# Optimization experiments

Hardware: AMD Instinct MI355X
Metric: run time of the kernel (lower is better)

Reference implementation:

```python
import jax, jax.numpy as jnp
import numpy as np

B, H, S, DK = 2, 16, 2048, 64


def setup_inputs() -> dict:
    key = jax.random.key(0)
    kq, kk, kv = jax.random.split(key, 3)
    query = jax.random.normal(kq, (B, H, S, DK), dtype=jnp.float32)
    k = jax.random.normal(kk, (B, H, S, DK), dtype=jnp.float32)
    value = jax.random.normal(kv, (B, H, S, DK), dtype=jnp.float32)
    # causal padding-style mask: 1 = keep, 0 = masked (set to -inf pre-softmax)
    mask = jnp.tril(jnp.ones((S, S), dtype=jnp.int32))[None, None, :, :]
    return {"query": query, "key": k, "value": value, "d_k": DK, "mask": mask}


def reference(query, key, value, d_k, mask):
    # scores: [B, H, Sq, Sk]
    scores = jnp.einsum("bhqd,bhkd->bhqk", query, key)
    scores = scores / jnp.sqrt(jnp.asarray(d_k, dtype=scores.dtype))
    scores = jnp.where(mask == 0, -jnp.inf, scores)
    att = jax.nn.softmax(scores, axis=-1)
    # dropout is identity in eval mode (deterministic reference)
    out = jnp.einsum("bhqk,bhkd->bhqd", att, value)
    return out
```

## Files before the change

kernel.cpp:

```cpp
#include <hip/hip_runtime.h>
#include <cstdint>

#define B_ 2
#define H_ 16
#define S_ 2048
#define DK_ 64
#define BH_ (B_*H_)
#define NQT 32

typedef __attribute__((ext_vector_type(8))) short short8;
typedef __attribute__((ext_vector_type(4))) float floatx4;
typedef __attribute__((ext_vector_type(16))) float floatx16;

__device__ inline unsigned short f2bf(float f) {
  union { float f; unsigned u; } v; v.f = f;
  unsigned u = v.u;
  unsigned r = u + 0x7fffu + ((u >> 16) & 1u);
  return (unsigned short)(r >> 16);
}

__device__ inline floatx16 mfma32(short8 a, short8 b, floatx16 c) {
  return __builtin_amdgcn_mfma_f32_32x32x16_bf16(a, b, c, 0, 0, 0);
}

__global__ __launch_bounds__(256) void conv_kv(const float* __restrict__ K,
                                               const float* __restrict__ V,
                                               unsigned short* __restrict__ Kb,
                                               unsigned short* __restrict__ Vb) {
  __shared__ __align__(16) unsigned short t[64 * 80];
  const int bh = blockIdx.y, s0 = blockIdx.x * 64;
  const int row = threadIdx.x >> 2, cp = threadIdx.x & 3;

  {
    const float* src = K + ((size_t)(bh * S_ + s0 + row)) * DK_ + cp * 16;
    unsigned short* dst = Kb + ((size_t)(bh * S_ + s0 + row)) * DK_ + cp * 16;
    #pragma unroll
    for (int h = 0; h < 2; ++h) {
      float4 a = *(const float4*)(src + h * 8);
      float4 b = *(const float4*)(src + h * 8 + 4);
      uint4 st;
      st.x = (unsigned)f2bf(a.x) | ((unsigned)f2bf(a.y) << 16);
      st.y = (unsigned)f2bf(a.z) | ((unsigned)f2bf(a.w) << 16);
      st.z = (unsigned)f2bf(b.x) | ((unsigned)f2bf(b.y) << 16);
      st.w = (unsigned)f2bf(b.z) | ((unsigned)f2bf(b.w) << 16);
      *(uint4*)(dst + h * 8) = st;
    }
  }
  {
    const float* src = V + ((size_t)(bh * S_ + s0 + row)) * DK_ + cp * 16;
    #pragma unroll
    for (int j4 = 0; j4 < 4; ++j4) {
      float4 a = *(const float4*)(src + j4 * 4);
      int c = cp * 16 + j4 * 4;
      t[(c + 0) * 80 + row] = f2bf(a.x);
      t[(c + 1) * 80 + row] = f2bf(a.y);
      t[(c + 2) * 80 + row] = f2bf(a.z);
      t[(c + 3) * 80 + row] = f2bf(a.w);
    }
    __syncthreads();
    unsigned short* dst = Vb + ((size_t)(bh * DK_ + row)) * S_ + s0 + cp * 16;
    *(uint4*)(dst + 0) = *(const uint4*)&t[row * 80 + cp * 16];
    *(uint4*)(dst + 8) = *(const uint4*)&t[row * 80 + cp * 16 + 8];
  }
}

__global__ __launch_bounds__(256, 4)
void fa_kernel(const float* __restrict__ Q, const unsigned short* __restrict__ Kb,
               const unsigned short* __restrict__ Vb, float* __restrict__ Out) {
  __shared__ __align__(16) unsigned short SMEM[2 * 8192 + 256];

  const int tid  = threadIdx.x;
  const int wave = tid >> 6;
  const int lane = tid & 63;
  const int l31  = lane & 31;
  const int h    = lane >> 5;
  const int wq   = wave >> 1;
  const int ws   = wave & 1;

  const int id = blockIdx.x;
  const int bh = id & 31;
  const int u  = id >> 5;
  const int r  = u & 7, k4 = u >> 3;
  const int qt = (k4 == 0) ? r : (k4 == 1) ? (15 - r) : (k4 == 2) ? (16 + r) : (31 - r);
  const int nkv = qt + 1;

  const float SCL = 0.125f * 1.44269504088896340736f;

  short8 qf[4];
  {
    const float* qp = Q + ((size_t)bh * S_ + qt * 64 + wq * 32 + l31) * DK_ + h * 8;
    #pragma unroll
    for (int dstep = 0; dstep < 4; ++dstep) {
      float4 x = *(const float4*)(qp + dstep * 16);
      float4 y = *(const float4*)(qp + dstep * 16 + 4);
      short8 t;
      t[0]=(short)f2bf(x.x*SCL); t[1]=(short)f2bf(x.y*SCL); t[2]=(short)f2bf(x.z*SCL); t[3]=(short)f2bf(x.w*SCL);
      t[4]=(short)f2bf(y.x*SCL); t[5]=(short)f2bf(y.y*SCL); t[6]=(short)f2bf(y.z*SCL); t[7]=(short)f2bf(y.w*SCL);
      qf[dstep] = t;
    }
  }

  floatx16 Ot[2] = { {0,0,0,0,0,0,0,0,0,0,0,0,0,0,0,0},
                     {0,0,0,0,0,0,0,0,0,0,0,0,0,0,0,0} };
  float ls = 0.f;

  auto stage = [&](int slot, int kv) {
    #pragma unroll
    for (int rd = 0; rd < 2; ++rd) {
      const int cid = rd * 256 + tid;
      const int row = cid >> 3;
      const int c   = (cid & 7) ^ (row & 7);
      {
        const unsigned short* g = Kb + (((size_t)bh * S_ + kv * 64 + row) << 6) + (c << 3);
        __builtin_amdgcn_global_load_lds(
            (const __attribute__((address_space(1))) void*)g,
            (__attribute__((address_space(3))) void*)&SMEM[slot * 8192 + rd * 2048 + wave * 512],
            16, 0, 0);
      }
      {
        const unsigned short* g = Vb + (((size_t)(bh * DK_ + row)) << 11) + kv * 64 + (c << 3);
        __builtin_amdgcn_global_load_lds(
            (const __attribute__((address_space(1))) void*)g,
            (__attribute__((address_space(3))) void*)&SMEM[slot * 8192 + 4096 + rd * 2048 + wave * 512],
            16, 0, 0);
      }
    }
  };

  auto computeT = [&](int cur, bool diag) {
    if (diag && wq == 0 && ws == 1) return;
    const unsigned short* Kt = SMEM + cur * 8192;
    const unsigned short* Vt = Kt + 4096;
    floatx16 s = {0,0,0,0,0,0,0,0,0,0,0,0,0,0,0,0};
    const int krow = ws * 32 + l31;
    #pragma unroll
    for (int dstep = 0; dstep < 4; ++dstep) {
      const short8 a = *(const short8*)&Kt[krow * 64 + (((dstep << 1) + h) ^ (krow & 7)) * 8];
      s = mfma32(a, qf[dstep], s);
    }
    if (diag && wq == ws) {
      #pragma unroll
      for (int rg = 0; rg < 16; ++rg) {
        const int sl = (rg & 3) + 8 * (rg >> 2) + 4 * h;
        if (sl > l31) s[rg] = -INFINITY;
      }
    }
    float e[16];
    #pragma unroll
    for (int i = 0; i < 16; ++i) e[i] = __builtin_amdgcn_exp2f(s[i]);
    ls += (((e[0]+e[1])+(e[2]+e[3])) + ((e[4]+e[5])+(e[6]+e[7])))
        + (((e[8]+e[9])+(e[10]+e[11])) + ((e[12]+e[13])+(e[14]+e[15])));
    short8 pb[2];
    #pragma unroll
    for (int t = 0; t < 2; ++t) {
      unsigned X0, X1, Y0, Y1;
      asm("v_cvt_pk_bf16_f32 %0, %1, %2" : "=v"(X0) : "v"(e[8*t+0]), "v"(e[8*t+1]));
      asm("v_cvt_pk_bf16_f32 %0, %1, %2" : "=v"(X1) : "v"(e[8*t+2]), "v"(e[8*t+3]));
      asm("v_cvt_pk_bf16_f32 %0, %1, %2" : "=v"(Y0) : "v"(e[8*t+4]), "v"(e[8*t+5]));
      asm("v_cvt_pk_bf16_f32 %0, %1, %2" : "=v"(Y1) : "v"(e[8*t+6]), "v"(e[8*t+7]));
      asm("v_permlane32_swap_b32 %0, %1" : "+v"(X0), "+v"(Y0));
      asm("v_permlane32_swap_b32 %0, %1" : "+v"(X1), "+v"(Y1));
      union { unsigned u[4]; short8 s8; } pbu;
      pbu.u[0] = X0; pbu.u[1] = X1; pbu.u[2] = Y0; pbu.u[3] = Y1;
      pb[t] = pbu.s8;
    }
    #pragma unroll
    for (int dsub = 0; dsub < 2; ++dsub) {
      const int vrow = dsub * 32 + l31;
      const short8 v0 = *(const short8*)&Vt[vrow * 64 + (((ws << 2) + h    ) ^ (vrow & 7)) * 8];
      const short8 v1 = *(const short8*)&Vt[vrow * 64 + (((ws << 2) + h + 2) ^ (vrow & 7)) * 8];
      Ot[dsub] = mfma32(v0, pb[0], Ot[dsub]);
      Ot[dsub] = mfma32(v1, pb[1], Ot[dsub]);
    }
  };

  stage(0, 0);
  for (int kv = 0; kv < nkv; ++kv) {
    asm volatile("s_waitcnt vmcnt(0)" ::: "memory");
    __builtin_amdgcn_s_barrier();
    if (kv + 1 < nkv) stage((kv + 1) & 1, kv + 1);
    computeT(kv & 1, kv == nkv - 1);
  }

  ls += __shfl_xor(ls, 32);
  float* OP = (float*)SMEM;
  float* LP = OP + 4096;
  __syncthreads();
  if (ws == 1) {
    #pragma unroll
    for (int dsub = 0; dsub < 2; ++dsub)
      #pragma unroll
      for (int rg = 0; rg < 16; ++rg)
        OP[((wq * 2 + dsub) * 16 + rg) * 64 + lane] = Ot[dsub][rg];
    LP[wq * 64 + lane] = ls;
  }
  __syncthreads();
  if (ws == 0) {
    const float inv = 1.0f / (ls + LP[wq * 64 + lane]);
    float* og = Out + ((size_t)(bh * S_ + qt * 64 + wq * 32 + l31)) * DK_;
    #pragma unroll
    for (int dsub = 0; dsub < 2; ++dsub) {
      #pragma unroll
      for (int g = 0; g < 4; ++g) {
        floatx4 o;
        #pragma unroll
        for (int j = 0; j < 4; ++j)
          o[j] = (Ot[dsub][4 * g + j] + OP[((wq * 2 + dsub) * 16 + 4 * g + j) * 64 + lane]) * inv;
        *(floatx4*)(og + dsub * 32 + 8 * g + 4 * h) = o;
      }
    }
  }
}

extern "C" void kernel_launch(void* const* d_in, const int* in_sizes, int n_in,
                              void* d_out, int out_size, void* d_ws, size_t ws_size,
                              hipStream_t stream) {
  const float* Q = (const float*)d_in[0];
  const float* K = (const float*)d_in[1];
  const float* V = (const float*)d_in[2];
  float* Out = (float*)d_out;
  unsigned short* Kb = (unsigned short*)d_ws;
  unsigned short* Vb = Kb + (size_t)BH_ * S_ * DK_;
  conv_kv<<<dim3(S_ / 64, BH_), 256, 0, stream>>>(K, V, Kb, Vb);
  fa_kernel<<<dim3(NQT * BH_), 256, 0, stream>>>(Q, Kb, Vb, Out);
}
```

Baseline: 131.9 us.

## Pair complementary causal query tiles per block to share K/V tile loads

Each workgroup now processes two query tiles (p and 31-p), so every block does the same amount of causal work, and the K/V tiles staged in LDS plus the fragments read from them are reused by both tiles. The change halves the grid, cuts global and LDS traffic for K/V per unit of work, and removes the imbalance between short and long causal rows. In exchange register pressure roughly doubles for the Q fragments and accumulators, so launch bounds drop to 2 blocks per CU. There are also only 512 blocks, which may leave the GPU with less latency hiding.

After: 131.7 us. Within noise of the previous version (-0.1%).

```diff
diff --git a/kernel.cpp b/kernel.cpp
--- a/kernel.cpp
+++ b/kernel.cpp
@@ -64,7 +64,7 @@
   }
 }
 
-__global__ __launch_bounds__(256, 4)
+__global__ __launch_bounds__(256, 2)
 void fa_kernel(const float* __restrict__ Q, const unsigned short* __restrict__ Kb,
                const unsigned short* __restrict__ Vb, float* __restrict__ Out) {
   __shared__ __align__(16) unsigned short SMEM[2 * 8192 + 256];
@@ -79,15 +79,14 @@
 
   const int id = blockIdx.x;
   const int bh = id & 31;
-  const int u  = id >> 5;
-  const int r  = u & 7, k4 = u >> 3;
-  const int qt = (k4 == 0) ? r : (k4 == 1) ? (15 - r) : (k4 == 2) ? (16 + r) : (31 - r);
-  const int nkv = qt + 1;
+  const int p  = id >> 5;
+  const int qa = p, qb = NQT - 1 - p;
+  const int nkvA = qa + 1, nkvB = qb + 1;
 
   const float SCL = 0.125f * 1.44269504088896340736f;
 
-  short8 qf[4];
-  {
+  short8 qfB[4], qfA[4];
+  auto loadQ = [&](int qt, short8* qf) {
     const float* qp = Q + ((size_t)bh * S_ + qt * 64 + wq * 32 + l31) * DK_ + h * 8;
     #pragma unroll
     for (int dstep = 0; dstep < 4; ++dstep) {
@@ -98,11 +97,15 @@
       t[4]=(short)f2bf(y.x*SCL); t[5]=(short)f2bf(y.y*SCL); t[6]=(short)f2bf(y.z*SCL); t[7]=(short)f2bf(y.w*SCL);
       qf[dstep] = t;
     }
-  }
-
-  floatx16 Ot[2] = { {0,0,0,0,0,0,0,0,0,0,0,0,0,0,0,0},
-                     {0,0,0,0,0,0,0,0,0,0,0,0,0,0,0,0} };
-  float ls = 0.f;
+  };
+  loadQ(qb, qfB);
+  loadQ(qa, qfA);
+
+  floatx16 OtB[2] = { {0,0,0,0,0,0,0,0,0,0,0,0,0,0,0,0},
+                      {0,0,0,0,0,0,0,0,0,0,0,0,0,0,0,0} };
+  floatx16 OtA[2] = { {0,0,0,0,0,0,0,0,0,0,0,0,0,0,0,0},
+                      {0,0,0,0,0,0,0,0,0,0,0,0,0,0,0,0} };
+  float lsB = 0.f, lsA = 0.f;
 
   auto stage = [&](int slot, int kv) {
     #pragma unroll
@@ -127,17 +130,12 @@
     }
   };
 
-  auto computeT = [&](int cur, bool diag) {
+  auto doTile = [&](const short8* ak, const short8 (*vf)[2], const short8* qf,
+                    floatx16* Ot, float& ls, bool diag) {
     if (diag && wq == 0 && ws == 1) return;
-    const unsigned short* Kt = SMEM + cur * 8192;
-    const unsigned short* Vt = Kt + 4096;
     floatx16 s = {0,0,0,0,0,0,0,0,0,0,0,0,0,0,0,0};
-    const int krow = ws * 32 + l31;
-    #pragma unroll
-    for (int dstep = 0; dstep < 4; ++dstep) {
-      const short8 a = *(const short8*)&Kt[krow * 64 + (((dstep << 1) + h) ^ (krow & 7)) * 8];
-      s = mfma32(a, qf[dstep], s);
-    }
+    #pragma unroll
+    for (int dstep = 0; dstep < 4; ++dstep) s = mfma32(ak[dstep], qf[dstep], s);
     if (diag && wq == ws) {
       #pragma unroll
       for (int rg = 0; rg < 16; ++rg) {
@@ -166,49 +164,70 @@
     }
     #pragma unroll
     for (int dsub = 0; dsub < 2; ++dsub) {
-      const int vrow = dsub * 32 + l31;
-      const short8 v0 = *(const short8*)&Vt[vrow * 64 + (((ws << 2) + h    ) ^ (vrow & 7)) * 8];
-      const short8 v1 = *(const short8*)&Vt[vrow * 64 + (((ws << 2) + h + 2) ^ (vrow & 7)) * 8];
-      Ot[dsub] = mfma32(v0, pb[0], Ot[dsub]);
-      Ot[dsub] = mfma32(v1, pb[1], Ot[dsub]);
+      Ot[dsub] = mfma32(vf[dsub][0], pb[0], Ot[dsub]);
+      Ot[dsub] = mfma32(vf[dsub][1], pb[1], Ot[dsub]);
     }
   };
 
   stage(0, 0);
-  for (int kv = 0; kv < nkv; ++kv) {
+  for (int kv = 0; kv < nkvB; ++kv) {
     asm volatile("s_waitcnt vmcnt(0)" ::: "memory");
     __builtin_amdgcn_s_barrier();
-    if (kv + 1 < nkv) stage((kv + 1) & 1, kv + 1);
-    computeT(kv & 1, kv == nkv - 1);
-  }
-
-  ls += __shfl_xor(ls, 32);
+    if (kv + 1 < nkvB) stage((kv + 1) & 1, kv + 1);
+    const unsigned short* Kt = SMEM + (kv & 1) * 8192;
+    const unsigned short* Vt = Kt + 4096;
+    short8 ak[4];
+    const int krow = ws * 32 + l31;
+    #pragma unroll
+    for (int dstep = 0; dstep < 4; ++dstep)
+      ak[dstep] = *(const short8*)&Kt[krow * 64 + (((dstep << 1) + h) ^ (krow & 7)) * 8];
+    short8 vf[2][2];
+    #pragma unroll
+    for (int dsub = 0; dsub < 2; ++dsub) {
+      const int vrow = dsub * 32 + l31;
+      vf[dsub][0] = *(const short8*)&Vt[vrow * 64 + (((ws << 2) + h    ) ^ (vrow & 7)) * 8];
+      vf[dsub][1] = *(const short8*)&Vt[vrow * 64 + (((ws << 2) + h + 2) ^ (vrow & 7)) * 8];
+    }
+    doTile(ak, vf, qfB, OtB, lsB, kv == nkvB - 1);
+    if (kv < nkvA) doTile(ak, vf, qfA, OtA, lsA, kv == nkvA - 1);
+  }
+
+  lsB += __shfl_xor(lsB, 32);
+  lsA += __shfl_xor(lsA, 32);
+
   float* OP = (float*)SMEM;
   float* LP = OP + 4096;
   __syncthreads();
-  if (ws == 1) {
-    #pragma unroll
-    for (int dsub = 0; dsub < 2; ++dsub)
+  #pragma unroll
+  for (int t = 0; t < 2; ++t) {
+    const floatx16* Ot = t ? OtA : OtB;
+    const float lsv    = t ? lsA : lsB;
+    const int qt       = t ? qa : qb;
+    if (ws == 1) {
       #pragma unroll
-      for (int rg = 0; rg < 16; ++rg)
-        OP[((wq * 2 + dsub) * 16 + rg) * 64 + lane] = Ot[dsub][rg];
-    LP[wq * 64 + lane] = ls;
-  }
-  __syncthreads();
-  if (ws == 0) {
-    const float inv = 1.0f / (ls + LP[wq * 64 + lane]);
-    float* og = Out + ((size_t)(bh * S_ + qt * 64 + wq * 32 + l31)) * DK_;
-    #pragma unroll
-    for (int dsub = 0; dsub < 2; ++dsub) {
+      for (int dsub = 0; dsub < 2; ++dsub)
+        #pragma unroll
+        for (int rg = 0; rg < 16; ++rg)
+          OP[((wq * 2 + dsub) * 16 + rg) * 64 + lane] = Ot[dsub][rg];
+      LP[wq * 64 + lane] = lsv;
+    }
+    __syncthreads();
+    if (ws == 0) {
+      const float inv = 1.0f / (lsv + LP[wq * 64 + lane]);
+      float* og = Out + ((size_t)(bh * S_ + qt * 64 + wq * 32 + l31)) * DK_;
       #pragma unroll
-      for (int g = 0; g < 4; ++g) {
-        floatx4 o;
+      for (int dsub = 0; dsub < 2; ++dsub) {
         #pragma unroll
-        for (int j = 0; j < 4; ++j)
-          o[j] = (Ot[dsub][4 * g + j] + OP[((wq * 2 + dsub) * 16 + 4 * g + j) * 64 + lane]) * inv;
-        *(floatx4*)(og + dsub * 32 + 8 * g + 4 * h) = o;
-      }
-    }
+        for (int g = 0; g < 4; ++g) {
+          floatx4 o;
+          #pragma unroll
+          for (int j = 0; j < 4; ++j)
+            o[j] = (Ot[dsub][4 * g + j] + OP[((wq * 2 + dsub) * 16 + 4 * g + j) * 64 + lane]) * inv;
+          *(floatx4*)(og + dsub * 32 + 8 * g + 4 * h) = o;
+        }
+      }
+    }
+    __syncthreads();
   }
 }
 
@@ -222,5 +241,5 @@
   unsigned short* Kb = (unsigned short*)d_ws;
   unsigned short* Vb = Kb + (size_t)BH_ * S_ * DK_;
   conv_kv<<<dim3(S_ / 64, BH_), 256, 0, stream>>>(K, V, Kb, Vb);
-  fa_kernel<<<dim3(NQT * BH_), 256, 0, stream>>>(Q, Kb, Vb, Out);
-}
+  fa_kernel<<<dim3((NQT / 2) * BH_), 256, 0, stream>>>(Q, Kb, Vb, Out);
+}
```
